# Kernel tuning notes

Measured on AMD Instinct MI355X. Metric: run time of the kernel, lower is better.

Reference implementation:

```python
import jax, jax.numpy as jnp
import numpy as np

FPS_RATIO = 0.1
K = 20
EPS = 1e-6
COS_EPS = 1e-8  # torch nn.CosineSimilarity default eps


def setup_inputs() -> dict:
    key = jax.random.key(0)
    k1, k2 = jax.random.split(key)
    N = 40000
    pos = jax.random.normal(k1, (N, 3), dtype=jnp.float32) * 10.0   # spatial coordinates
    vec_pred = jax.random.normal(k2, (N, 3), dtype=jnp.float32)     # predicted direction vectors
    return {"vec_pred": vec_pred, "pos": pos}


def _fps(pos, n_anchors):
    """Deterministic farthest point sampling starting from point 0. Returns [n_anchors] int32."""
    d0 = jnp.sum((pos - pos[0]) ** 2, axis=-1)  # [N]
    def body(min_d, _):
        idx = jnp.argmax(min_d)
        d = jnp.sum((pos - pos[idx]) ** 2, axis=-1)
        return jnp.minimum(min_d, d), idx.astype(jnp.int32)
    _, idxs = jax.lax.scan(body, d0, None, length=n_anchors - 1)
    return jnp.concatenate([jnp.zeros((1,), jnp.int32), idxs])


def _vec_loss(vec_pred, pos):
    N = pos.shape[0]
    n_anchors = int(np.ceil(FPS_RATIO * N))
    anchors = _fps(pos, n_anchors)
    anchors_pos = pos[anchors]                                     # [A, 3]
    # Brute-force KNN: squared distances anchors -> all points, [A, N]
    d2 = (jnp.sum(anchors_pos ** 2, -1, keepdims=True)
          - 2.0 * anchors_pos @ pos.T
          + jnp.sum(pos ** 2, -1)[None, :])
    _, nn_idx = jax.lax.top_k(-d2, K)                              # [A, K]
    nbhds = pos[nn_idx]                                            # [A, K, 3]
    # pca_lowrank: center then SVD; principal direction = top right singular vector
    centered = nbhds - jnp.mean(nbhds, axis=1, keepdims=True)
    _, _, vh = jnp.linalg.svd(centered, full_matrices=False)       # vh: [A, 3, 3]
    vecs = vh[:, 0, :]                                             # [A, 3]
    # Faithful to original: index[0] (anchor ids, each repeated K times) indexes BOTH tensors
    idx0 = jnp.repeat(jnp.arange(n_anchors), K)                    # [A*K]
    a = vec_pred[idx0]
    b = vecs[idx0]
    denom = (jnp.maximum(jnp.linalg.norm(a, axis=-1), COS_EPS)
             * jnp.maximum(jnp.linalg.norm(b, axis=-1), COS_EPS))
    abs_cos = jnp.abs(jnp.sum(a * b, axis=-1) / denom)
    return -jnp.mean(jnp.log(abs_cos + EPS))


def reference(vec_pred, pos):
    # single graph -> forward's average over graphs is just this scalar
    return _vec_loss(vec_pred, pos)
```

## Files before the change

kernel.cpp:

```cpp
#include <hip/hip_runtime.h>
#include <math.h>

#define N_PTS       40000
#define N_ANCH      4000
#define KNN         20
#define NB          32
#define BT          256
#define NWAVES      128
#define STRIDE      (NB * BT)
#define PPT         5
#define TW          4
#define POOL        (NWAVES * TW)
#define RSLOTS      (POOL / 64)
#define CCAP        6

typedef unsigned long long ull;

#define LD_RLX(p)    __hip_atomic_load((p),  __ATOMIC_RELAXED, __HIP_MEMORY_SCOPE_AGENT)
#define ST_REL(p,v)  __hip_atomic_store((p), (v), __ATOMIC_RELEASE, __HIP_MEMORY_SCOPE_AGENT)
#define ST_RLX(p,v)  __hip_atomic_store((p), (v), __ATOMIC_RELAXED, __HIP_MEMORY_SCOPE_AGENT)


__device__ __forceinline__ double dist64(double px, double py, double pz,
                                         double wx, double wy, double wz) {
  double dx = px - wx, dy = py - wy, dz = pz - wz;
  return dx * dx + dy * dy + dz * dz;
}

__device__ __forceinline__ unsigned key32(double v) {
  unsigned hi = (unsigned)__double2hiint(v);
  return (hi & 0x80000000u) ? ~hi : (hi | 0x80000000u);
}

__device__ __forceinline__ unsigned wave_umax_dpp(unsigned x) {
#define DPP_STEP(ctrl) { unsigned y = (unsigned)__builtin_amdgcn_update_dpp( \
      0, (int)x, ctrl, 0xf, 0xf, true); x = (y > x) ? y : x; }
  DPP_STEP(0x111)
  DPP_STEP(0x112)
  DPP_STEP(0x114)
  DPP_STEP(0x118)
  DPP_STEP(0x142)
  DPP_STEP(0x143)
#undef DPP_STEP
  return (unsigned)__builtin_amdgcn_readlane((int)x, 63);
}

__device__ __forceinline__ int rl_i(int v, int l) { return __builtin_amdgcn_readlane(v, l); }
__device__ __forceinline__ double rl_d(double v, int l) {
  int lo = __builtin_amdgcn_readlane(__double2loint(v), l);
  int hi = __builtin_amdgcn_readlane(__double2hiint(v), l);
  return __hiloint2double(hi, lo);
}

__device__ __forceinline__ void wave_argmax_exact(double& wv, int& wix) {
#pragma unroll
  for (int off = 1; off < 64; off <<= 1) {
    double ov = __shfl_xor(wv, off);
    int    oi = __shfl_xor(wix, off);
    bool bt = (ov > wv) || (ov == wv && oi < wix);
    wv = bt ? ov : wv; wix = bt ? oi : wix;
  }
}

__device__ __forceinline__ void wave_pick(double v, int idx,
                                          unsigned& wkey, int& wlane, int& widx) {
  unsigned k = key32(v);
  unsigned M = wave_umax_dpp(k);
  ull mask = __ballot(k == M);
  if (__popcll(mask) == 1) {
    wlane = __ffsll(mask) - 1;
    widx  = rl_i(idx, wlane);
    wkey  = M;
  } else {
    double wv = v; int wi = idx;
    wave_argmax_exact(wv, wi);
    widx = wi;
    wkey = key32(wv);
    ull m2 = __ballot(idx == widx);
    wlane = __ffsll(m2) - 1;
  }
}

struct FpsSm {
  double lv[4][384];
  float  lc[4][384][3];
  int    li[4][384];
};
struct KnnSm { ull m4[4]; ull g; int w[KNN]; int ai; };
union Smem { FpsSm f; KnnSm k; };

__device__ static inline void eig3_maxvec(double xx, double xy, double xz,
                                          double yy, double yz, double zz,
                                          double& v0, double& v1, double& v2) {
  double q  = (xx + yy + zz) / 3.0;
  double p1 = xy * xy + xz * xz + yz * yz;
  double a00 = xx - q, a11 = yy - q, a22 = zz - q;
  double p2 = a00 * a00 + a11 * a11 + a22 * a22 + 2.0 * p1;
  if (p2 < 1e-300) { v0 = 1.0; v1 = 0.0; v2 = 0.0; return; }
  double p   = sqrt(p2 / 6.0);
  double inv = 1.0 / p;
  double b00 = a00 * inv, b01 = xy * inv, b02 = xz * inv;
  double b11 = a11 * inv, b12 = yz * inv, b22 = a22 * inv;
  double detB = b00 * (b11 * b22 - b12 * b12)
              - b01 * (b01 * b22 - b12 * b02)
              + b02 * (b01 * b12 - b11 * b02);
  double r = fmin(1.0, fmax(-1.0, detB * 0.5));
  double phi = acos(r) / 3.0;
  double lam = q + 2.0 * p * cos(phi);

  double r0x = xx - lam, r0y = xy,       r0z = xz;
  double r1x = xy,       r1y = yy - lam, r1z = yz;
  double r2x = xz,       r2y = yz,       r2z = zz - lam;
  double c0x = r0y * r1z - r0z * r1y, c0y = r0z * r1x - r0x * r1z, c0z = r0x * r1y - r0y * r1x;
  double c1x = r0y * r2z - r0z * r2y, c1y = r0z * r2x - r0x * r2z, c1z = r0x * r2y - r0y * r2x;
  double c2x = r1y * r2z - r1z * r2y, c2y = r1z * r2x - r1x * r2z, c2z = r1x * r2y - r1y * r2x;
  double n0 = c0x * c0x + c0y * c0y + c0z * c0z;
  double n1 = c1x * c1x + c1y * c1y + c1z * c1z;
  double n2 = c2x * c2x + c2y * c2y + c2z * c2z;
  double bx = c0x, by = c0y, bz = c0z, bn = n0;
  if (n1 > bn) { bx = c1x; by = c1y; bz = c1z; bn = n1; }
  if (n2 > bn) { bx = c2x; by = c2y; bz = c2z; bn = n2; }
  if (bn < 1e-280) { v0 = 1.0; v1 = 0.0; v2 = 0.0; return; }
  double s = 1.0 / sqrt(bn);
  v0 = bx * s; v1 = by * s; v2 = bz * s;
}

__global__ __launch_bounds__(BT, 2) void fps_knn_kernel(
    const float* __restrict__ pos, const float* __restrict__ vec_pred,
    int* __restrict__ flag, ull* __restrict__ slots,
    int* __restrict__ anchors, double* __restrict__ acc) {
  __shared__ Smem sm;
  const int t    = threadIdx.x;
  const int lane = t & 63;
  const int wave = t >> 6;

  if (blockIdx.x < NB) {
    const int b    = blockIdx.x;
    const int gtid = b * BT + t;
    const int gw   = b * 4 + wave;

    double pdx[PPT], pdy[PPT], pdz[PPT], md[PPT];
    const double a0x = (double)pos[0], a0y = (double)pos[1], a0z = (double)pos[2];
#pragma unroll
    for (int k = 0; k < PPT; ++k) {
      int i = gtid + k * STRIDE;
      if (i < N_PTS) {
        pdx[k] = (double)pos[3 * i];
        pdy[k] = (double)pos[3 * i + 1];
        pdz[k] = (double)pos[3 * i + 2];
        md[k]  = dist64(pdx[k], pdy[k], pdz[k], a0x, a0y, a0z);
      } else {
        pdx[k] = 0.0; pdy[k] = 0.0; pdz[k] = 0.0;
        md[k]  = -1.0e300;
      }
    }
    if (b == 0 && t == 0) ST_RLX(anchors + 0, 0);

    double bv = -1.0e301; int bi = 0x7fffffff;
#pragma unroll
    for (int k = 0; k < PPT; ++k) {
      int i = gtid + k * STRIDE;
      bool bt = (md[k] > bv) || (md[k] == bv && i < bi);
      bv = bt ? md[k] : bv; bi = bt ? i : bi;
    }

    int nsel  = 1;
    int batch = 0;
#pragma unroll 1
    while (nsel < N_ANCH) {
      batch++;
      const int par = batch & 1;

      unsigned cons = 0;
      double pv = -1.0e301; int pix = 0;
#pragma unroll 1
      for (int r = 0; r < TW; ++r) {
        unsigned wkey; int wlane, widx;
        wave_pick(bv, bi, wkey, wlane, widx);
        double wval = rl_d(bv, wlane);
        if (lane == wlane && bi != 0x7fffffff) {
          cons |= 1u << ((unsigned)(bi - gtid) >> 13);
          bv = -1.0e301; bi = 0x7fffffff;
#pragma unroll
          for (int k = 0; k < PPT; ++k) {
            if (!((cons >> k) & 1u)) {
              int i = gtid + k * STRIDE;
              bool bt = (md[k] > bv) || (md[k] == bv && i < bi);
              bv = bt ? md[k] : bv; bi = bt ? i : bi;
            }
          }
        }
        if (lane == r) { pv = wval; pix = widx; }
      }

      if (lane < TW) {
        ull* sp = slots + (ull)((par * POOL + gw * TW + lane) * 2);
        ST_RLX(sp,     (ull)__double_as_longlong(pv));
        ST_RLX(sp + 1, (ull)(unsigned)pix);
      }
      if (lane == 0) ST_REL(flag + gw, batch);

      for (;;) {
        int f0 = LD_RLX(flag + lane);
        int f1 = LD_RLX(flag + 64 + lane);
        if (__ballot((f0 >= batch) && (f1 >= batch)) == ~0ull) break;
        __builtin_amdgcn_s_sleep(1);
      }
      __builtin_amdgcn_sched_barrier(0);

      double cv[RSLOTS]; int ci[RSLOTS];
#pragma unroll
      for (int j = 0; j < RSLOTS; ++j) {
        ull* sp = slots + (ull)((par * POOL + lane + 64 * j) * 2);
        cv[j] = __longlong_as_double((long long)LD_RLX(sp));
        ci[j] = (int)(unsigned)LD_RLX(sp + 1);
      }

      unsigned kj[RSLOTS];
      unsigned lkmax = 0;
#pragma unroll
      for (int j = 0; j < RSLOTS; ++j) {
        kj[j] = key32(cv[j]);
        lkmax = (kj[j] > lkmax) ? kj[j] : lkmax;
      }
      const unsigned Mkey    = wave_umax_dpp(lkmax);
      const unsigned BmaxKey = wave_umax_dpp(((lane & 3) == 3) ? lkmax : 0u);

      int cap = N_ANCH - nsel;
      int S = 0;

      if (Mkey > BmaxKey) {
        int base = 0;
#pragma unroll
        for (int j = 0; j < RSLOTS; ++j) {
          bool live = kj[j] > BmaxKey;
          ull bal = __ballot(live);
          int rank = base + __popcll(bal & ((1ull << lane) - 1ull));
          if (live) {
            sm.f.lv[wave][rank] = cv[j];
            sm.f.li[wave][rank] = ci[j];
            int p = ci[j];
            sm.f.lc[wave][rank][0] = pos[3 * p];
            sm.f.lc[wave][rank][1] = pos[3 * p + 1];
            sm.f.lc[wave][rank][2] = pos[3 * p + 2];
          }
          base += (int)__popcll(bal);
        }
        const int live_n = base;

        double cv2[CCAP], c2x[CCAP], c2y[CCAP], c2z[CCAP]; int ci2[CCAP];
#pragma unroll
        for (int tt = 0; tt < CCAP; ++tt) {
          if (live_n > tt * 64) {
            int e = tt * 64 + lane;
            bool ok = e < live_n;
            double v = sm.f.lv[wave][e];
            int    ii = sm.f.li[wave][e];
            float  x = sm.f.lc[wave][e][0];
            float  y = sm.f.lc[wave][e][1];
            float  z = sm.f.lc[wave][e][2];
            cv2[tt] = ok ? v : -1.0e301;
            ci2[tt] = ok ? ii : 0x7fffffff;
            c2x[tt] = ok ? (double)x : 0.0;
            c2y[tt] = ok ? (double)y : 0.0;
            c2z[tt] = ok ? (double)z : 0.0;
          } else {
            cv2[tt] = -1.0e301; ci2[tt] = 0x7fffffff;
            c2x[tt] = 0.0; c2y[tt] = 0.0; c2z[tt] = 0.0;
          }
        }

#pragma unroll 1
        while (S < cap) {
          double wv = cv2[0]; int wix = ci2[0];
          double fx = c2x[0], fy = c2y[0], fz = c2z[0];
#pragma unroll
          for (int tt = 1; tt < CCAP; ++tt) {
            if (live_n > tt * 64) {
              bool bt = (cv2[tt] > wv) || (cv2[tt] == wv && ci2[tt] < wix);
              wv = bt ? cv2[tt] : wv; wix = bt ? ci2[tt] : wix;
              fx = bt ? c2x[tt] : fx; fy = bt ? c2y[tt] : fy; fz = bt ? c2z[tt] : fz;
            }
          }
          unsigned wkey; int wlane, widx;
          wave_pick(wv, wix, wkey, wlane, widx);
          if (S != 0 && !(wkey > BmaxKey)) break;
          double wxd = rl_d(fx, wlane), wyd = rl_d(fy, wlane), wzd = rl_d(fz, wlane);
          if (gw == 0 && lane == 0) ST_RLX(anchors + nsel + S, widx);
#pragma unroll
          for (int tt = 0; tt < CCAP; ++tt) {
            if (live_n > tt * 64) {
              cv2[tt] = fmin(cv2[tt], dist64(c2x[tt], c2y[tt], c2z[tt], wxd, wyd, wzd));
              if (ci2[tt] == widx) cv2[tt] = -1.0e301;
            }
          }
#pragma unroll
          for (int k = 0; k < PPT; ++k)
            md[k] = fmin(md[k], dist64(pdx[k], pdy[k], pdz[k], wxd, wyd, wzd));
          S++;
        }
      } else {
#pragma unroll 1
        while (S < cap) {
          double wv = cv[0]; int wix = ci[0];
#pragma unroll
          for (int j = 1; j < RSLOTS; ++j) {
            bool bt = (cv[j] > wv) || (cv[j] == wv && ci[j] < wix);
            wv = bt ? cv[j] : wv; wix = bt ? ci[j] : wix;
          }
          unsigned wkey; int wlane, widx;
          wave_pick(wv, wix, wkey, wlane, widx);
          if (S != 0 && !(wkey > BmaxKey)) break;
          double wxd = (double)pos[3 * widx];
          double wyd = (double)pos[3 * widx + 1];
          double wzd = (double)pos[3 * widx + 2];
          if (gw == 0 && lane == 0) ST_RLX(anchors + nsel + S, widx);
#pragma unroll
          for (int j = 0; j < RSLOTS; ++j) {
            int p = ci[j];
            double d = dist64((double)pos[3 * p], (double)pos[3 * p + 1],
                              (double)pos[3 * p + 2], wxd, wyd, wzd);
            cv[j] = fmin(cv[j], d);
            if (ci[j] == widx) cv[j] = -1.0e301;
          }
#pragma unroll
          for (int k = 0; k < PPT; ++k)
            md[k] = fmin(md[k], dist64(pdx[k], pdy[k], pdz[k], wxd, wyd, wzd));
          S++;
        }
      }
      nsel += S;

      bv = -1.0e301; bi = 0x7fffffff;
#pragma unroll
      for (int k = 0; k < PPT; ++k) {
        int i = gtid + k * STRIDE;
        bool bt = (md[k] > bv) || (md[k] == bv && i < bi);
        bv = bt ? md[k] : bv; bi = bt ? i : bi;
      }
    }
  } else {
    const int aidx = blockIdx.x - NB;
    if (t == 0) {
      int a = LD_RLX(anchors + aidx);
      int spin = 1;
      while (a < 0) {
        for (int u = 0; u < spin; ++u) __builtin_amdgcn_s_sleep(32);
        if (spin < 32) spin <<= 1;
        a = LD_RLX(anchors + aidx);
      }
      sm.k.ai = a;
    }
    __syncthreads();
    const int ai = sm.k.ai;
    const float ax = pos[3 * ai], ay = pos[3 * ai + 1], az = pos[3 * ai + 2];

    ull key[KNN];
#pragma unroll
    for (int s = 0; s < KNN; ++s) key[s] = ~0ull;
    ull kmax = ~0ull; int smax = 0;
#pragma unroll 1
    for (int k = 0; k < (N_PTS + BT - 1) / BT; ++k) {
      int j = k * BT + t;
      if (j < N_PTS) {
        float dx = pos[3 * j] - ax, dy = pos[3 * j + 1] - ay, dz = pos[3 * j + 2] - az;
        float d  = dx * dx + dy * dy + dz * dz;
        ull nk = ((ull)__float_as_uint(d) << 32) | (unsigned)j;
        if (nk < kmax) {
#pragma unroll
          for (int s = 0; s < KNN; ++s) key[s] = (s == smax) ? nk : key[s];
          kmax = 0ull; smax = 0;
#pragma unroll
          for (int s = 0; s < KNN; ++s) {
            bool g = key[s] > kmax;
            kmax = g ? key[s] : kmax;
            smax = g ? s : smax;
          }
        }
      }
    }

    ull lmin = ~0ull; int ls = 0;
#pragma unroll
    for (int s = 0; s < KNN; ++s) {
      bool l = key[s] < lmin;
      lmin = l ? key[s] : lmin; ls = l ? s : ls;
    }
#pragma unroll 1
    for (int r = 0; r < KNN; ++r) {
      ull mv = lmin;
#pragma unroll
      for (int off = 32; off >= 1; off >>= 1) {
        ull ov = __shfl_down(mv, off);
        mv = (ov < mv) ? ov : mv;
      }
      if (lane == 0) sm.k.m4[wave] = mv;
      __syncthreads();
      if (t == 0) {
        ull g = sm.k.m4[0];
#pragma unroll
        for (int w = 1; w < 4; ++w) g = (sm.k.m4[w] < g) ? sm.k.m4[w] : g;
        sm.k.g = g;
        sm.k.w[r] = (int)(g & 0xffffffffull);
      }
      __syncthreads();
      ull g = sm.k.g;
      if (lmin == g) {
#pragma unroll
        for (int s = 0; s < KNN; ++s) key[s] = (s == ls) ? ~0ull : key[s];
        lmin = ~0ull; ls = 0;
#pragma unroll
        for (int s = 0; s < KNN; ++s) {
          bool l = key[s] < lmin;
          lmin = l ? key[s] : lmin; ls = l ? s : ls;
        }
      }
    }

    if (t == 0) {
      double mx = 0, my = 0, mz = 0;
      for (int r = 0; r < KNN; ++r) {
        int p = sm.k.w[r];
        mx += (double)pos[3 * p]; my += (double)pos[3 * p + 1]; mz += (double)pos[3 * p + 2];
      }
      mx /= KNN; my /= KNN; mz /= KNN;
      double xx = 0, xy = 0, xz = 0, yy = 0, yz = 0, zz = 0;
      for (int r = 0; r < KNN; ++r) {
        int p = sm.k.w[r];
        double cx = (double)pos[3 * p]     - mx;
        double cy = (double)pos[3 * p + 1] - my;
        double cz = (double)pos[3 * p + 2] - mz;
        xx += cx * cx; xy += cx * cy; xz += cx * cz;
        yy += cy * cy; yz += cy * cz; zz += cz * cz;
      }
      double v0, v1, v2;
      eig3_maxvec(xx, xy, xz, yy, yz, zz, v0, v1, v2);

      double a0 = vec_pred[3 * aidx], a1 = vec_pred[3 * aidx + 1], a2 = vec_pred[3 * aidx + 2];
      double an = sqrt(a0 * a0 + a1 * a1 + a2 * a2);
      double bn = sqrt(v0 * v0 + v1 * v1 + v2 * v2);
      double denom = fmax(an, 1e-8) * fmax(bn, 1e-8);
      double c = fabs((a0 * v0 + a1 * v1 + a2 * v2) / denom);
      atomicAdd(acc, log(c + 1e-6));
    }
  }
}

__global__ void finalize_kernel(const double* __restrict__ acc, float* __restrict__ out) {
  out[0] = (float)(-acc[0] / (double)N_ANCH);
}

extern "C" void kernel_launch(void* const* d_in, const int* in_sizes, int n_in,
                              void* d_out, int out_size, void* d_ws, size_t ws_size,
                              hipStream_t stream) {
  (void)in_sizes; (void)n_in; (void)out_size; (void)ws_size;
  const float* vec_pred = (const float*)d_in[0];
  const float* pos      = (const float*)d_in[1];
  float* out = (float*)d_out;

  char* ws = (char*)d_ws;
  double* acc     = (double*)(ws + 0);
  int*    flag    = (int*)(ws + 64);
  ull*    slots   = (ull*)(ws + 1024);
  int*    anchors = (int*)(ws + 17408);

  hipMemsetAsync(ws, 0, 1024, stream);
  hipMemsetAsync(ws + 17408, 0xFF, N_ANCH * 4, stream);
  hipLaunchKernelGGL(fps_knn_kernel, dim3(NB + N_ANCH), dim3(BT), 0, stream,
                     pos, vec_pred, flag, slots, anchors, acc);
  hipLaunchKernelGGL(finalize_kernel, dim3(1), dim3(1), 0, stream, acc, out);
}
```

Before: 3.313 ms.

## Elect one wave per block for FPS candidate selection and share winners via LDS

```diff
diff --git a/kernel.cpp b/kernel.cpp
--- a/kernel.cpp
+++ b/kernel.cpp
@@ -13,6 +13,7 @@
 #define POOL        (NWAVES * TW)
 #define RSLOTS      (POOL / 64)
 #define CCAP        6
+#define SCAP        384
 
 typedef unsigned long long ull;
 
@@ -82,9 +83,11 @@
 }
 
 struct FpsSm {
-  double lv[4][384];
-  float  lc[4][384][3];
-  int    li[4][384];
+  union {
+    struct { double lv[SCAP]; double lc[SCAP][3]; int li[SCAP]; } c;
+    struct { double wc[SCAP][3]; int wi[SCAP]; } w;
+  } u;
+  int Scount;
 };
 struct KnnSm { ull m4[4]; ull g; int w[KNN]; int ai; };
 union Smem { FpsSm f; KnnSm k; };
@@ -138,6 +141,7 @@
     const int b    = blockIdx.x;
     const int gtid = b * BT + t;
     const int gw   = b * 4 + wave;
+    const int sel  = b & 3;
 
     double pdx[PPT], pdy[PPT], pdz[PPT], md[PPT];
     const double a0x = (double)pos[0], a0y = (double)pos[1], a0z = (double)pos[2];
@@ -200,134 +204,151 @@
       }
       if (lane == 0) ST_REL(flag + gw, batch);
 
-      for (;;) {
-        int f0 = LD_RLX(flag + lane);
-        int f1 = LD_RLX(flag + 64 + lane);
-        if (__ballot((f0 >= batch) && (f1 >= batch)) == ~0ull) break;
-        __builtin_amdgcn_s_sleep(1);
-      }
-      __builtin_amdgcn_sched_barrier(0);
-
-      double cv[RSLOTS]; int ci[RSLOTS];
-#pragma unroll
-      for (int j = 0; j < RSLOTS; ++j) {
-        ull* sp = slots + (ull)((par * POOL + lane + 64 * j) * 2);
-        cv[j] = __longlong_as_double((long long)LD_RLX(sp));
-        ci[j] = (int)(unsigned)LD_RLX(sp + 1);
-      }
-
-      unsigned kj[RSLOTS];
-      unsigned lkmax = 0;
-#pragma unroll
-      for (int j = 0; j < RSLOTS; ++j) {
-        kj[j] = key32(cv[j]);
-        lkmax = (kj[j] > lkmax) ? kj[j] : lkmax;
-      }
-      const unsigned Mkey    = wave_umax_dpp(lkmax);
-      const unsigned BmaxKey = wave_umax_dpp(((lane & 3) == 3) ? lkmax : 0u);
-
-      int cap = N_ANCH - nsel;
-      int S = 0;
-
-      if (Mkey > BmaxKey) {
-        int base = 0;
+      if (wave == sel) {
+        for (;;) {
+          int f0 = LD_RLX(flag + lane);
+          int f1 = LD_RLX(flag + 64 + lane);
+          if (__ballot((f0 >= batch) && (f1 >= batch)) == ~0ull) break;
+          __builtin_amdgcn_s_sleep(1);
+        }
+        __builtin_amdgcn_sched_barrier(0);
+
+        double cv[RSLOTS]; int ci[RSLOTS];
 #pragma unroll
         for (int j = 0; j < RSLOTS; ++j) {
-          bool live = kj[j] > BmaxKey;
-          ull bal = __ballot(live);
-          int rank = base + __popcll(bal & ((1ull << lane) - 1ull));
-          if (live) {
-            sm.f.lv[wave][rank] = cv[j];
-            sm.f.li[wave][rank] = ci[j];
-            int p = ci[j];
-            sm.f.lc[wave][rank][0] = pos[3 * p];
-            sm.f.lc[wave][rank][1] = pos[3 * p + 1];
-            sm.f.lc[wave][rank][2] = pos[3 * p + 2];
-          }
-          base += (int)__popcll(bal);
-        }
-        const int live_n = base;
-
-        double cv2[CCAP], c2x[CCAP], c2y[CCAP], c2z[CCAP]; int ci2[CCAP];
-#pragma unroll
-        for (int tt = 0; tt < CCAP; ++tt) {
-          if (live_n > tt * 64) {
-            int e = tt * 64 + lane;
-            bool ok = e < live_n;
-            double v = sm.f.lv[wave][e];
-            int    ii = sm.f.li[wave][e];
-            float  x = sm.f.lc[wave][e][0];
-            float  y = sm.f.lc[wave][e][1];
-            float  z = sm.f.lc[wave][e][2];
-            cv2[tt] = ok ? v : -1.0e301;
-            ci2[tt] = ok ? ii : 0x7fffffff;
-            c2x[tt] = ok ? (double)x : 0.0;
-            c2y[tt] = ok ? (double)y : 0.0;
-            c2z[tt] = ok ? (double)z : 0.0;
-          } else {
-            cv2[tt] = -1.0e301; ci2[tt] = 0x7fffffff;
-            c2x[tt] = 0.0; c2y[tt] = 0.0; c2z[tt] = 0.0;
-          }
-        }
-
-#pragma unroll 1
-        while (S < cap) {
-          double wv = cv2[0]; int wix = ci2[0];
-          double fx = c2x[0], fy = c2y[0], fz = c2z[0];
-#pragma unroll
-          for (int tt = 1; tt < CCAP; ++tt) {
-            if (live_n > tt * 64) {
-              bool bt = (cv2[tt] > wv) || (cv2[tt] == wv && ci2[tt] < wix);
-              wv = bt ? cv2[tt] : wv; wix = bt ? ci2[tt] : wix;
-              fx = bt ? c2x[tt] : fx; fy = bt ? c2y[tt] : fy; fz = bt ? c2z[tt] : fz;
-            }
-          }
-          unsigned wkey; int wlane, widx;
-          wave_pick(wv, wix, wkey, wlane, widx);
-          if (S != 0 && !(wkey > BmaxKey)) break;
-          double wxd = rl_d(fx, wlane), wyd = rl_d(fy, wlane), wzd = rl_d(fz, wlane);
-          if (gw == 0 && lane == 0) ST_RLX(anchors + nsel + S, widx);
+          ull* sp = slots + (ull)((par * POOL + lane + 64 * j) * 2);
+          cv[j] = __longlong_as_double((long long)LD_RLX(sp));
+          ci[j] = (int)(unsigned)LD_RLX(sp + 1);
+        }
+
+        unsigned kj[RSLOTS];
+        unsigned lkmax = 0;
+#pragma unroll
+        for (int j = 0; j < RSLOTS; ++j) {
+          kj[j] = key32(cv[j]);
+          lkmax = (kj[j] > lkmax) ? kj[j] : lkmax;
+        }
+        const unsigned Mkey    = wave_umax_dpp(lkmax);
+        const unsigned BmaxKey = wave_umax_dpp(((lane & 3) == 3) ? lkmax : 0u);
+
+        int cap = N_ANCH - nsel; if (cap > SCAP) cap = SCAP;
+        int S = 0;
+
+        if (Mkey > BmaxKey) {
+          int base = 0;
+#pragma unroll
+          for (int j = 0; j < RSLOTS; ++j) {
+            bool live = kj[j] > BmaxKey;
+            ull bal = __ballot(live);
+            int rank = base + (int)__popcll(bal & ((1ull << lane) - 1ull));
+            if (live) {
+              sm.f.u.c.lv[rank] = cv[j];
+              sm.f.u.c.li[rank] = ci[j];
+              int p = ci[j];
+              sm.f.u.c.lc[rank][0] = (double)pos[3 * p];
+              sm.f.u.c.lc[rank][1] = (double)pos[3 * p + 1];
+              sm.f.u.c.lc[rank][2] = (double)pos[3 * p + 2];
+            }
+            base += (int)__popcll(bal);
+          }
+          const int live_n = base;
+
+          double cv2[CCAP], c2x[CCAP], c2y[CCAP], c2z[CCAP]; int ci2[CCAP];
 #pragma unroll
           for (int tt = 0; tt < CCAP; ++tt) {
             if (live_n > tt * 64) {
-              cv2[tt] = fmin(cv2[tt], dist64(c2x[tt], c2y[tt], c2z[tt], wxd, wyd, wzd));
-              if (ci2[tt] == widx) cv2[tt] = -1.0e301;
-            }
-          }
-#pragma unroll
-          for (int k = 0; k < PPT; ++k)
-            md[k] = fmin(md[k], dist64(pdx[k], pdy[k], pdz[k], wxd, wyd, wzd));
-          S++;
-        }
-      } else {
-#pragma unroll 1
-        while (S < cap) {
-          double wv = cv[0]; int wix = ci[0];
-#pragma unroll
-          for (int j = 1; j < RSLOTS; ++j) {
-            bool bt = (cv[j] > wv) || (cv[j] == wv && ci[j] < wix);
-            wv = bt ? cv[j] : wv; wix = bt ? ci[j] : wix;
-          }
-          unsigned wkey; int wlane, widx;
-          wave_pick(wv, wix, wkey, wlane, widx);
-          if (S != 0 && !(wkey > BmaxKey)) break;
-          double wxd = (double)pos[3 * widx];
-          double wyd = (double)pos[3 * widx + 1];
-          double wzd = (double)pos[3 * widx + 2];
-          if (gw == 0 && lane == 0) ST_RLX(anchors + nsel + S, widx);
-#pragma unroll
-          for (int j = 0; j < RSLOTS; ++j) {
-            int p = ci[j];
-            double d = dist64((double)pos[3 * p], (double)pos[3 * p + 1],
-                              (double)pos[3 * p + 2], wxd, wyd, wzd);
-            cv[j] = fmin(cv[j], d);
-            if (ci[j] == widx) cv[j] = -1.0e301;
-          }
-#pragma unroll
-          for (int k = 0; k < PPT; ++k)
-            md[k] = fmin(md[k], dist64(pdx[k], pdy[k], pdz[k], wxd, wyd, wzd));
-          S++;
-        }
+              int e = tt * 64 + lane;
+              bool ok = e < live_n;
+              double v  = sm.f.u.c.lv[e];
+              int    ii = sm.f.u.c.li[e];
+              double x  = sm.f.u.c.lc[e][0];
+              double y  = sm.f.u.c.lc[e][1];
+              double z  = sm.f.u.c.lc[e][2];
+              cv2[tt] = ok ? v : -1.0e301;
+              ci2[tt] = ok ? ii : 0x7fffffff;
+              c2x[tt] = ok ? x : 0.0;
+              c2y[tt] = ok ? y : 0.0;
+              c2z[tt] = ok ? z : 0.0;
+            } else {
+              cv2[tt] = -1.0e301; ci2[tt] = 0x7fffffff;
+              c2x[tt] = 0.0; c2y[tt] = 0.0; c2z[tt] = 0.0;
+            }
+          }
+
+#pragma unroll 1
+          while (S < cap) {
+            double wv = cv2[0]; int wix = ci2[0];
+            double fx = c2x[0], fy = c2y[0], fz = c2z[0];
+#pragma unroll
+            for (int tt = 1; tt < CCAP; ++tt) {
+              if (live_n > tt * 64) {
+                bool bt = (cv2[tt] > wv) || (cv2[tt] == wv && ci2[tt] < wix);
+                wv = bt ? cv2[tt] : wv; wix = bt ? ci2[tt] : wix;
+                fx = bt ? c2x[tt] : fx; fy = bt ? c2y[tt] : fy; fz = bt ? c2z[tt] : fz;
+              }
+            }
+            unsigned wkey; int wlane, widx;
+            wave_pick(wv, wix, wkey, wlane, widx);
+            if (S != 0 && !(wkey > BmaxKey)) break;
+            double wxd = rl_d(fx, wlane), wyd = rl_d(fy, wlane), wzd = rl_d(fz, wlane);
+            if (lane == 0) {
+              sm.f.u.w.wc[S][0] = wxd; sm.f.u.w.wc[S][1] = wyd; sm.f.u.w.wc[S][2] = wzd;
+              sm.f.u.w.wi[S] = widx;
+              if (b == 0) ST_RLX(anchors + nsel + S, widx);
+            }
+#pragma unroll
+            for (int tt = 0; tt < CCAP; ++tt) {
+              if (live_n > tt * 64) {
+                cv2[tt] = fmin(cv2[tt], dist64(c2x[tt], c2y[tt], c2z[tt], wxd, wyd, wzd));
+                if (ci2[tt] == widx) cv2[tt] = -1.0e301;
+              }
+            }
+            S++;
+          }
+        } else {
+#pragma unroll 1
+          while (S < cap) {
+            double wv = cv[0]; int wix = ci[0];
+#pragma unroll
+            for (int j = 1; j < RSLOTS; ++j) {
+              bool bt = (cv[j] > wv) || (cv[j] == wv && ci[j] < wix);
+              wv = bt ? cv[j] : wv; wix = bt ? ci[j] : wix;
+            }
+            unsigned wkey; int wlane, widx;
+            wave_pick(wv, wix, wkey, wlane, widx);
+            if (S != 0 && !(wkey > BmaxKey)) break;
+            double wxd = (double)pos[3 * widx];
+            double wyd = (double)pos[3 * widx + 1];
+            double wzd = (double)pos[3 * widx + 2];
+            if (lane == 0) {
+              sm.f.u.w.wc[S][0] = wxd; sm.f.u.w.wc[S][1] = wyd; sm.f.u.w.wc[S][2] = wzd;
+              sm.f.u.w.wi[S] = widx;
+              if (b == 0) ST_RLX(anchors + nsel + S, widx);
+            }
+#pragma unroll
+            for (int j = 0; j < RSLOTS; ++j) {
+              int p = ci[j];
+              double d = dist64((double)pos[3 * p], (double)pos[3 * p + 1],
+                                (double)pos[3 * p + 2], wxd, wyd, wzd);
+              cv[j] = fmin(cv[j], d);
+              if (ci[j] == widx) cv[j] = -1.0e301;
+            }
+            S++;
+          }
+        }
+        if (lane == 0) sm.f.Scount = S;
+      }
+      __syncthreads();
+
+      const int S = sm.f.Scount;
+#pragma unroll 1
+      for (int s = 0; s < S; ++s) {
+        double wx = sm.f.u.w.wc[s][0];
+        double wy = sm.f.u.w.wc[s][1];
+        double wz = sm.f.u.w.wc[s][2];
+#pragma unroll
+        for (int k = 0; k < PPT; ++k)
+          md[k] = fmin(md[k], dist64(pdx[k], pdy[k], pdz[k], wx, wy, wz));
       }
       nsel += S;
 
```

Measured after the change: 3.499 ms. 5.6% more time.

## Switch to single-wave blocks for FPS and KNN, drop block-level syncs

Applied to the files above, without the earlier changes.

```diff
diff --git a/kernel.cpp b/kernel.cpp
--- a/kernel.cpp
+++ b/kernel.cpp
@@ -4,10 +4,10 @@
 #define N_PTS       40000
 #define N_ANCH      4000
 #define KNN         20
-#define NB          32
-#define BT          256
+#define NFB         128
+#define BT          64
 #define NWAVES      128
-#define STRIDE      (NB * BT)
+#define STRIDE      (NWAVES * 64)
 #define PPT         5
 #define TW          4
 #define POOL        (NWAVES * TW)
@@ -82,11 +82,11 @@
 }
 
 struct FpsSm {
-  double lv[4][384];
-  float  lc[4][384][3];
-  int    li[4][384];
+  double lv[CCAP * 64];
+  float  lc[CCAP * 64][3];
+  int    li[CCAP * 64];
 };
-struct KnnSm { ull m4[4]; ull g; int w[KNN]; int ai; };
+struct KnnSm { int w[KNN]; };
 union Smem { FpsSm f; KnnSm k; };
 
 __device__ static inline void eig3_maxvec(double xx, double xy, double xz,
@@ -130,14 +130,11 @@
     int* __restrict__ flag, ull* __restrict__ slots,
     int* __restrict__ anchors, double* __restrict__ acc) {
   __shared__ Smem sm;
-  const int t    = threadIdx.x;
-  const int lane = t & 63;
-  const int wave = t >> 6;
-
-  if (blockIdx.x < NB) {
-    const int b    = blockIdx.x;
-    const int gtid = b * BT + t;
-    const int gw   = b * 4 + wave;
+  const int lane = threadIdx.x & 63;
+
+  if (blockIdx.x < NFB) {
+    const int gw   = blockIdx.x;
+    const int gtid = gw * 64 + lane;
 
     double pdx[PPT], pdy[PPT], pdz[PPT], md[PPT];
     const double a0x = (double)pos[0], a0y = (double)pos[1], a0z = (double)pos[2];
@@ -154,7 +151,7 @@
         md[k]  = -1.0e300;
       }
     }
-    if (b == 0 && t == 0) ST_RLX(anchors + 0, 0);
+    if (gw == 0 && lane == 0) ST_RLX(anchors + 0, 0);
 
     double bv = -1.0e301; int bi = 0x7fffffff;
 #pragma unroll
@@ -235,14 +232,14 @@
         for (int j = 0; j < RSLOTS; ++j) {
           bool live = kj[j] > BmaxKey;
           ull bal = __ballot(live);
-          int rank = base + __popcll(bal & ((1ull << lane) - 1ull));
+          int rank = base + (int)__popcll(bal & ((1ull << lane) - 1ull));
           if (live) {
-            sm.f.lv[wave][rank] = cv[j];
-            sm.f.li[wave][rank] = ci[j];
+            sm.f.lv[rank] = cv[j];
+            sm.f.li[rank] = ci[j];
             int p = ci[j];
-            sm.f.lc[wave][rank][0] = pos[3 * p];
-            sm.f.lc[wave][rank][1] = pos[3 * p + 1];
-            sm.f.lc[wave][rank][2] = pos[3 * p + 2];
+            sm.f.lc[rank][0] = pos[3 * p];
+            sm.f.lc[rank][1] = pos[3 * p + 1];
+            sm.f.lc[rank][2] = pos[3 * p + 2];
           }
           base += (int)__popcll(bal);
         }
@@ -254,11 +251,11 @@
           if (live_n > tt * 64) {
             int e = tt * 64 + lane;
             bool ok = e < live_n;
-            double v = sm.f.lv[wave][e];
-            int    ii = sm.f.li[wave][e];
-            float  x = sm.f.lc[wave][e][0];
-            float  y = sm.f.lc[wave][e][1];
-            float  z = sm.f.lc[wave][e][2];
+            double v  = sm.f.lv[e];
+            int    ii = sm.f.li[e];
+            float  x  = sm.f.lc[e][0];
+            float  y  = sm.f.lc[e][1];
+            float  z  = sm.f.lc[e][2];
             cv2[tt] = ok ? v : -1.0e301;
             ci2[tt] = ok ? ii : 0x7fffffff;
             c2x[tt] = ok ? (double)x : 0.0;
@@ -340,19 +337,15 @@
       }
     }
   } else {
-    const int aidx = blockIdx.x - NB;
-    if (t == 0) {
-      int a = LD_RLX(anchors + aidx);
-      int spin = 1;
-      while (a < 0) {
-        for (int u = 0; u < spin; ++u) __builtin_amdgcn_s_sleep(32);
-        if (spin < 32) spin <<= 1;
-        a = LD_RLX(anchors + aidx);
-      }
-      sm.k.ai = a;
-    }
-    __syncthreads();
-    const int ai = sm.k.ai;
+    const int aidx = blockIdx.x - NFB;
+    int a = -1;
+    for (;;) {
+      if (lane == 0) a = LD_RLX(anchors + aidx);
+      a = __shfl(a, 0);
+      if (a >= 0) break;
+      __builtin_amdgcn_s_sleep(32);
+    }
+    const int ai = a;
     const float ax = pos[3 * ai], ay = pos[3 * ai + 1], az = pos[3 * ai + 2];
 
     ull key[KNN];
@@ -360,22 +353,20 @@
     for (int s = 0; s < KNN; ++s) key[s] = ~0ull;
     ull kmax = ~0ull; int smax = 0;
 #pragma unroll 1
-    for (int k = 0; k < (N_PTS + BT - 1) / BT; ++k) {
-      int j = k * BT + t;
-      if (j < N_PTS) {
-        float dx = pos[3 * j] - ax, dy = pos[3 * j + 1] - ay, dz = pos[3 * j + 2] - az;
-        float d  = dx * dx + dy * dy + dz * dz;
-        ull nk = ((ull)__float_as_uint(d) << 32) | (unsigned)j;
-        if (nk < kmax) {
-#pragma unroll
-          for (int s = 0; s < KNN; ++s) key[s] = (s == smax) ? nk : key[s];
-          kmax = 0ull; smax = 0;
-#pragma unroll
-          for (int s = 0; s < KNN; ++s) {
-            bool g = key[s] > kmax;
-            kmax = g ? key[s] : kmax;
-            smax = g ? s : smax;
-          }
+    for (int k = 0; k < N_PTS / 64; ++k) {
+      int j = (k << 6) + lane;
+      float dx = pos[3 * j] - ax, dy = pos[3 * j + 1] - ay, dz = pos[3 * j + 2] - az;
+      float d  = dx * dx + dy * dy + dz * dz;
+      ull nk = ((ull)__float_as_uint(d) << 32) | (unsigned)j;
+      if (nk < kmax) {
+#pragma unroll
+        for (int s = 0; s < KNN; ++s) key[s] = (s == smax) ? nk : key[s];
+        kmax = 0ull; smax = 0;
+#pragma unroll
+        for (int s = 0; s < KNN; ++s) {
+          bool g = key[s] > kmax;
+          kmax = g ? key[s] : kmax;
+          smax = g ? s : smax;
         }
       }
     }
@@ -388,23 +379,13 @@
     }
 #pragma unroll 1
     for (int r = 0; r < KNN; ++r) {
-      ull mv = lmin;
-#pragma unroll
-      for (int off = 32; off >= 1; off >>= 1) {
-        ull ov = __shfl_down(mv, off);
-        mv = (ov < mv) ? ov : mv;
-      }
-      if (lane == 0) sm.k.m4[wave] = mv;
-      __syncthreads();
-      if (t == 0) {
-        ull g = sm.k.m4[0];
-#pragma unroll
-        for (int w = 1; w < 4; ++w) g = (sm.k.m4[w] < g) ? sm.k.m4[w] : g;
-        sm.k.g = g;
-        sm.k.w[r] = (int)(g & 0xffffffffull);
-      }
-      __syncthreads();
-      ull g = sm.k.g;
+      ull g = lmin;
+#pragma unroll
+      for (int off = 1; off < 64; off <<= 1) {
+        ull ov = __shfl_xor(g, off);
+        g = (ov < g) ? ov : g;
+      }
+      if (lane == 0) sm.k.w[r] = (int)(g & 0xffffffffull);
       if (lmin == g) {
 #pragma unroll
         for (int s = 0; s < KNN; ++s) key[s] = (s == ls) ? ~0ull : key[s];
@@ -417,7 +398,7 @@
       }
     }
 
-    if (t == 0) {
+    if (lane == 0) {
       double mx = 0, my = 0, mz = 0;
       for (int r = 0; r < KNN; ++r) {
         int p = sm.k.w[r];
@@ -466,7 +447,7 @@
 
   hipMemsetAsync(ws, 0, 1024, stream);
   hipMemsetAsync(ws + 17408, 0xFF, N_ANCH * 4, stream);
-  hipLaunchKernelGGL(fps_knn_kernel, dim3(NB + N_ANCH), dim3(BT), 0, stream,
+  hipLaunchKernelGGL(fps_knn_kernel, dim3(NFB + N_ANCH), dim3(BT), 0, stream,
                      pos, vec_pred, flag, slots, anchors, acc);
   hipLaunchKernelGGL(finalize_kernel, dim3(1), dim3(1), 0, stream, acc, out);
 }
```

After: 3.206 ms. 1.03x faster.
